# Kernel optimization log

Hardware: AMD Instinct MI355X
Metric: run time of the kernel (lower is better)

## Reference

```python
import jax, jax.numpy as jnp
import numpy as np
import math

B, S, D_IN, EMBED, H = 4, 1024, 1024, 1024, 16
HD = EMBED // H  # 64


def setup_inputs() -> dict:
    key = jax.random.key(0)
    ks = jax.random.split(key, 8)
    x = jax.random.normal(ks[0], (B, S, D_IN), dtype=jnp.float32)
    mask = jax.random.randint(ks[1], (B, S, S), 0, 2, dtype=jnp.int32)
    weights = jax.random.uniform(ks[2], (B, S, S), dtype=jnp.float32)
    # xavier-uniform-ish scale for projections
    lim_qkv = math.sqrt(6.0 / (D_IN + 3 * EMBED))
    lim_o = math.sqrt(6.0 / (EMBED + EMBED))
    W_qkv = jax.random.uniform(ks[3], (3 * EMBED, D_IN), minval=-lim_qkv, maxval=lim_qkv, dtype=jnp.float32)
    b_qkv = jnp.zeros((3 * EMBED,), dtype=jnp.float32)
    W_o = jax.random.uniform(ks[4], (EMBED, EMBED), minval=-lim_o, maxval=lim_o, dtype=jnp.float32)
    b_o = jnp.zeros((EMBED,), dtype=jnp.float32)
    return {"x": x, "mask": mask, "weights": weights, "W_qkv": W_qkv, "b_qkv": b_qkv, "W_o": W_o, "b_o": b_o}


def reference(x, mask, weights, W_qkv, b_qkv, W_o, b_o):
    b, s, _ = x.shape
    # QKV projection: [b, s, 3*EMBED] -> [b, H, s, 3*HD]
    qkv = (x @ W_qkv.T + b_qkv).reshape(b, s, H, 3 * HD).transpose(0, 2, 1, 3)
    q, k, v = jnp.split(qkv, 3, axis=-1)  # each [b, H, s, HD]
    logits = jnp.einsum('bhqd,bhkd->bhqk', q, k) / math.sqrt(HD)
    logits = jnp.where(mask[:, None, :, :] == 0, jnp.float32(-9e15), logits)
    # weights transposed on last two dims, broadcast over heads
    w = jnp.swapaxes(weights, -2, -1)[:, None, :, :]  # [b, 1, s, s]
    m = jnp.max(logits, axis=-1, keepdims=True)
    e = w * jnp.exp(logits - m)
    attn = e / jnp.sum(e, axis=-1, keepdims=True)
    vals = jnp.einsum('bhqk,bhkd->bhqd', attn, v)
    vals = vals.transpose(0, 2, 1, 3).reshape(b, s, EMBED)
    return vals @ W_o.T + b_o
```

## Files before the change

### kernel.cpp

```cpp
#include <hip/hip_runtime.h>
#include <hip/hip_bf16.h>
#include <stdint.h>

#define SDIM 1024
#define BATCH 4
#define NH 16
#define HDIM 64
#define KDIM 1024
#define N_QKV 3072
#define EMB 1024

typedef uint16_t u16;
typedef __attribute__((ext_vector_type(4))) float f32x4;
typedef __attribute__((ext_vector_type(8))) short bf16x8;
typedef __attribute__((ext_vector_type(8))) unsigned short u16x8;

__device__ __forceinline__ u16 f2bf(float f) {
  union { float f; uint32_t u; } x; x.f = f;
  uint32_t r = x.u + 0x7FFFu + ((x.u >> 16) & 1u);
  return (u16)(r >> 16);
}

__device__ __forceinline__ float bf2f(u16 b) {
  union { uint32_t u; float f; } x; x.u = ((uint32_t)b) << 16;
  return x.f;
}

__device__ __forceinline__ void gload_lds16(const u16* g, u16* l) {
  __builtin_amdgcn_global_load_lds(
      (const __attribute__((address_space(1))) unsigned int*)g,
      (__attribute__((address_space(3))) unsigned int*)l, 16, 0, 0);
}

#define N8_X  524288
#define N8_WQ 393216
#define N8_WO 131072
#define NCVT  1048576
#define NWM3  262144
__global__ void prep_kernel(const float* __restrict__ a, const float* __restrict__ bq,
                            const float* __restrict__ co,
                            u16* __restrict__ oa, u16* __restrict__ ob, u16* __restrict__ oc,
                            const int* __restrict__ mask, const float* __restrict__ wts,
                            u16* __restrict__ wm3) {
  const int total = NCVT + NWM3;
  const size_t SS = (size_t)SDIM * SDIM;
  int stride = gridDim.x * blockDim.x;
  for (int i = blockIdx.x * blockDim.x + threadIdx.x; i < total; i += stride) {
    if (i < NCVT) {
      const float* s; u16* d; int j;
      if (i < N8_X)             { s = a;  d = oa; j = i; }
      else if (i < N8_X + N8_WQ){ s = bq; d = ob; j = i - N8_X; }
      else                      { s = co; d = oc; j = i - N8_X - N8_WQ; }
      const float4* s4 = (const float4*)s + (size_t)j * 2;
      float4 u = s4[0], v = s4[1];
      u16x8 o;
      o[0] = f2bf(u.x); o[1] = f2bf(u.y); o[2] = f2bf(u.z); o[3] = f2bf(u.w);
      o[4] = f2bf(v.x); o[5] = f2bf(v.y); o[6] = f2bf(v.z); o[7] = f2bf(v.w);
      ((u16x8*)d)[j] = o;
    } else {
      int t = i - NCVT;
      int lane = t & 63, kt = (t >> 6) & 15, T = (t >> 10) & 63, b = t >> 16;
      int g2 = lane >> 4, c2 = lane & 15;
      int q = T * 16 + c2;
      const int* mrow = mask + (size_t)b * SS + (size_t)q * SDIM;
      const float* wcol = wts + (size_t)b * SS + q;
      u16* dst = wm3 + ((size_t)(b * 64 + T) * 16 + kt) * 1024 + lane * 16;
      #pragma unroll
      for (int hf = 0; hf < 2; ++hf) {
        int bk = kt * 64 + 8 * g2 + 32 * hf;
        int4 m0 = *(const int4*)(mrow + bk);
        int4 m1 = *(const int4*)(mrow + bk + 4);
        int mm[8] = {m0.x, m0.y, m0.z, m0.w, m1.x, m1.y, m1.z, m1.w};
        u16x8 o;
        #pragma unroll
        for (int e = 0; e < 8; ++e)
          o[e] = mm[e] ? f2bf(wcol[(size_t)(bk + e) * SDIM]) : (u16)0;
        *(u16x8*)(dst + hf * 8) = o;
      }
    }
  }
}

__global__ __launch_bounds__(512, 1) void gemm_qkv(
    const u16* __restrict__ A, const u16* __restrict__ Bm,
    const float* __restrict__ bias,
    u16* __restrict__ Qh, u16* __restrict__ Kh, u16* __restrict__ Vt)
{
  __shared__ char smem[114688];
  const int tid = threadIdx.x;
  const int gid = blockIdx.x;
  const int brow = (gid & 15) * 256, bcol = (gid >> 4) * 192;
  const int wid = tid >> 6, lane = tid & 63;
  const int g = lane >> 4, c = lane & 15, cx = c & 7;
  const int wr = wid & 3, wc = wid >> 2;

  const u16* asrc[4]; int adoff[4];
  #pragma unroll
  for (int j = 0; j < 4; ++j) {
    int i = j * 512 + tid;
    int row = i >> 3, sch = (i & 7) ^ (row & 7);
    asrc[j] = A + (size_t)(brow + row) * KDIM + sch * 8;
    adoff[j] = (j * 512 + wid * 64) * 16;
  }
  const u16* bsrc[3]; int bdoff[3];
  #pragma unroll
  for (int j = 0; j < 3; ++j) {
    int i = j * 512 + tid;
    int row = i >> 3, sch = (i & 7) ^ (row & 7);
    bsrc[j] = Bm + (size_t)(bcol + row) * KDIM + sch * 8;
    bdoff[j] = 32768 + (j * 512 + wid * 64) * 16;
  }

  auto stage = [&](int kt, int slot) {
    char* base = smem + slot * 57344;
    #pragma unroll
    for (int j = 0; j < 4; ++j)
      gload_lds16(asrc[j] + kt * 64, (u16*)(base + adoff[j]));
    #pragma unroll
    for (int j = 0; j < 3; ++j)
      gload_lds16(bsrc[j] + kt * 64, (u16*)(base + bdoff[j]));
  };

  f32x4 acc[4][6] = {};

  stage(0, 0);
  __syncthreads();

  for (int kt = 0; kt < 16; ++kt) {
    if (kt < 15) stage(kt + 1, (kt + 1) & 1);

    const char* As = smem + (kt & 1) * 57344;
    const char* Bs = As + 32768;

    #pragma unroll
    for (int kk = 0; kk < 2; ++kk) {
      bf16x8 af[4], bfr[6];
      #pragma unroll
      for (int m = 0; m < 4; ++m) {
        int row = wr * 64 + m * 16 + c;
        af[m] = *(const bf16x8*)(As + (row << 7) + ((((kk << 2) + g) ^ cx) << 4));
      }
      #pragma unroll
      for (int n = 0; n < 6; ++n) {
        int row = wc * 96 + n * 16 + c;
        bfr[n] = *(const bf16x8*)(Bs + (row << 7) + ((((kk << 2) + g) ^ cx) << 4));
      }
      __builtin_amdgcn_s_setprio(1);
      #pragma unroll
      for (int m = 0; m < 4; ++m)
        #pragma unroll
        for (int n = 0; n < 6; ++n)
          acc[m][n] = __builtin_amdgcn_mfma_f32_16x16x32_bf16(
              af[m], bfr[n], acc[m][n], 0, 0, 0);
      __builtin_amdgcn_s_setprio(0);
    }
    __syncthreads();
  }

  #pragma unroll
  for (int m = 0; m < 4; ++m) {
    #pragma unroll
    for (int n = 0; n < 6; ++n) {
      int col = bcol + wc * 96 + n * 16 + c;
      float bv = bias[col];
      int h = col / 192;
      int rem = col - h * 192;
      int sec = rem >> 6, d = rem & 63;
      #pragma unroll
      for (int r = 0; r < 4; ++r) {
        int row = brow + wr * 64 + m * 16 + g * 4 + r;
        int b = row >> 10, sl = row & 1023;
        float v = acc[m][n][r] + bv;
        if (sec == 0)
          Qh[((size_t)(b * NH + h) * SDIM + sl) * HDIM + d] = f2bf(v * 0.18033688f);
        else if (sec == 1)
          Kh[((size_t)(b * NH + h) * SDIM + sl) * HDIM + d] = f2bf(v);
        else
          Vt[((size_t)(b * NH + h) * HDIM + d) * SDIM + sl] = f2bf(v);
      }
    }
  }
}

__global__ __launch_bounds__(256) void gemm_bt(
    const u16* __restrict__ A, const u16* __restrict__ Bm,
    const float* __restrict__ bias, float* __restrict__ C,
    int M, int N, int K)
{
  __shared__ u16 As[128 * 64];
  __shared__ u16 Bs[128 * 64];
  const int tid = threadIdx.x;
  int bid = blockIdx.x;
  int swz = (bid & 7) * 32 + (bid >> 3);
  const int brow = (swz & 31) * 128, bcol = (swz >> 5) * 128;
  const int wid = tid >> 6, lane = tid & 63;
  const int g = lane >> 4, c = lane & 15, cx = c & 7;
  const int wrow = (wid >> 1) * 64, wcol = (wid & 1) * 64;

  const u16* asrc[4]; const u16* bsrc[4]; u16* adst[4]; u16* bdst[4];
  #pragma unroll
  for (int j = 0; j < 4; ++j) {
    int ci = j * 256 + tid;
    int row = ci >> 3, sch = (ci & 7) ^ (row & 7);
    asrc[j] = A  + (size_t)(brow + row) * K + sch * 8;
    bsrc[j] = Bm + (size_t)(bcol + row) * K + sch * 8;
    adst[j] = As + (j * 256 + wid * 64) * 8;
    bdst[j] = Bs + (j * 256 + wid * 64) * 8;
  }

  f32x4 acc[4][4] = {};
  const char* Asc = (const char*)As;
  const char* Bsc = (const char*)Bs;

  for (int kt = 0; kt < K / 64; ++kt) {
    #pragma unroll
    for (int j = 0; j < 4; ++j) {
      gload_lds16(asrc[j] + kt * 64, adst[j]);
      gload_lds16(bsrc[j] + kt * 64, bdst[j]);
    }
    __syncthreads();

    bf16x8 af[2][4], bfr[2][4];
    #pragma unroll
    for (int kk = 0; kk < 2; ++kk)
      #pragma unroll
      for (int i = 0; i < 4; ++i) {
        int cha = ((kk << 2) + g) ^ cx;
        af[kk][i]  = *(const bf16x8*)(Asc + ((wrow + i * 16 + c) << 7) + (cha << 4));
        bfr[kk][i] = *(const bf16x8*)(Bsc + ((wcol + i * 16 + c) << 7) + (cha << 4));
      }
    #pragma unroll
    for (int kk = 0; kk < 2; ++kk)
      #pragma unroll
      for (int mi = 0; mi < 4; ++mi)
        #pragma unroll
        for (int ni = 0; ni < 4; ++ni)
          acc[mi][ni] = __builtin_amdgcn_mfma_f32_16x16x32_bf16(
              af[kk][mi], bfr[kk][ni], acc[mi][ni], 0, 0, 0);
    __syncthreads();
  }

  #pragma unroll
  for (int mi = 0; mi < 4; ++mi)
    #pragma unroll
    for (int ni = 0; ni < 4; ++ni) {
      int col = bcol + wcol + ni * 16 + c;
      float bv = bias[col];
      #pragma unroll
      for (int r = 0; r < 4; ++r) {
        int row = brow + wrow + mi * 16 + g * 4 + r;
        C[(size_t)row * N + col] = acc[mi][ni][r] + bv;
      }
    }
}

__global__ __launch_bounds__(256, 4) void attn_kernel(
    const u16* __restrict__ Qh, const u16* __restrict__ Kh, const u16* __restrict__ Vt,
    const u16* __restrict__ wm3, u16* __restrict__ vals)
{
  int bid = blockIdx.x;
  int swz = (bid & 7) * 128 + (bid >> 3);
  const int qt = swz & 15, bh = swz >> 4;
  const int h = bh & 15, b = bh >> 4;

  const int tid = threadIdx.x;
  const int wid = tid >> 6, lane = tid & 63;
  const int g = lane >> 4, c = lane & 15;
  const int qloc = qt * 64 + wid * 16;

  __shared__ u16 Kb[2][4096];
  __shared__ u16 Vb[2][4096];

  const u16* qp = Qh + ((size_t)bh * SDIM + qloc + c) * HDIM;
  bf16x8 qa0 = *(const bf16x8*)(qp + g * 8);
  bf16x8 qa1 = *(const bf16x8*)(qp + 32 + g * 8);

  const u16* kbase = Kh + (size_t)bh * SDIM * HDIM;
  const u16* vbase = Vt + (size_t)bh * HDIM * SDIM;
  const u16* wbase = wm3 + (((size_t)(b * 16 + qt) * 4 + wid) * 16) * 1024 + lane * 16;

  float l_run = 0.f;
  f32x4 acc_o[4] = {};

  auto fsw = [](int row) { return ((row ^ (row >> 3)) & 7) ^ ((row & 1) << 2); };

  int kro[4], kxr[4], vro[4], vxr[4];
  #pragma unroll
  for (int st = 0; st < 4; ++st) {
    int kr = ((c >> 2) << 3) + ((st & 1) << 2) + (c & 3) + ((st >> 1) << 5);
    kro[st] = kr << 7;
    kxr[st] = fsw(kr);
  }
  #pragma unroll
  for (int dt = 0; dt < 4; ++dt) {
    int vr = dt * 16 + c;
    vro[dt] = vr << 7;
    vxr[dt] = fsw(vr);
  }

  auto stage = [&](int buf, int kt) {
    const int k0 = kt * 64;
    #pragma unroll
    for (int j = 0; j < 2; ++j) {
      int i = j * 256 + tid;
      int row = i >> 3;
      int sch = (i & 7) ^ (((row ^ (row >> 3)) & 7) ^ ((row & 1) << 2));
      gload_lds16(kbase + (size_t)(k0 + row) * HDIM + sch * 8,
                  &Kb[buf][(size_t)(j * 256 + wid * 64) * 8]);
      gload_lds16(vbase + (size_t)row * SDIM + k0 + sch * 8,
                  &Vb[buf][(size_t)(j * 256 + wid * 64) * 8]);
    }
  };

  stage(0, 0);
  __syncthreads();
  int cur = 0;

  for (int kt = 0; kt < 16; ++kt) {
    if (kt < 15) stage(cur ^ 1, kt + 1);

    u16x8 w0 = *(const u16x8*)(wbase + kt * 1024);
    u16x8 w1 = *(const u16x8*)(wbase + kt * 1024 + 8);

    const char* kb = (const char*)&Kb[cur][0];
    const char* vb = (const char*)&Vb[cur][0];

    f32x4 sc[4];
    #pragma unroll
    for (int st = 0; st < 4; ++st) {
      bf16x8 ka0 = *(const bf16x8*)(kb + kro[st] + ((g ^ kxr[st]) << 4));
      bf16x8 ka1 = *(const bf16x8*)(kb + kro[st] + (((4 + g) ^ kxr[st]) << 4));
      f32x4 z = {};
      z = __builtin_amdgcn_mfma_f32_16x16x32_bf16(ka0, qa0, z, 0, 0, 0);
      z = __builtin_amdgcn_mfma_f32_16x16x32_bf16(ka1, qa1, z, 0, 0, 0);
      sc[st] = z;
    }

    float p[4][4];
    #pragma unroll
    for (int st = 0; st < 4; ++st) {
      #pragma unroll
      for (int r = 0; r < 4; ++r) {
        u16 wv = (st < 2) ? ((const u16*)&w0)[st * 4 + r]
                          : ((const u16*)&w1)[(st - 2) * 4 + r];
        float pv = bf2f(wv) * __builtin_amdgcn_exp2f(sc[st][r]);
        p[st][r] = pv;
        l_run += pv;
      }
    }

    uint32_t pk[8];
    #pragma unroll
    for (int i = 0; i < 8; ++i) {
      float lo = p[i >> 1][(i & 1) * 2], hi = p[i >> 1][(i & 1) * 2 + 1];
      asm("v_cvt_pk_bf16_f32 %0, %1, %2" : "=v"(pk[i]) : "v"(lo), "v"(hi));
    }
    union PA { uint32_t u[4]; bf16x8 v; } a0, a1;
    #pragma unroll
    for (int i = 0; i < 4; ++i) { a0.u[i] = pk[i]; a1.u[i] = pk[4 + i]; }

    #pragma unroll
    for (int dt = 0; dt < 4; ++dt) {
      bf16x8 vb0 = *(const bf16x8*)(vb + vro[dt] + ((g ^ vxr[dt]) << 4));
      bf16x8 vb1 = *(const bf16x8*)(vb + vro[dt] + (((4 + g) ^ vxr[dt]) << 4));
      acc_o[dt] = __builtin_amdgcn_mfma_f32_16x16x32_bf16(a0.v, vb0, acc_o[dt], 0, 0, 0);
      acc_o[dt] = __builtin_amdgcn_mfma_f32_16x16x32_bf16(a1.v, vb1, acc_o[dt], 0, 0, 0);
    }

    __syncthreads();
    cur ^= 1;
  }

  l_run += __shfl_xor(l_run, 16);
  l_run += __shfl_xor(l_run, 32);

  float inv[4];
  #pragma unroll
  for (int r = 0; r < 4; ++r)
    inv[r] = 1.0f / __shfl(l_run, g * 4 + r);

  #pragma unroll
  for (int dt = 0; dt < 4; ++dt)
    #pragma unroll
    for (int r = 0; r < 4; ++r) {
      int row = b * SDIM + qloc + g * 4 + r;
      vals[(size_t)row * EMB + h * HDIM + dt * 16 + c] = f2bf(acc_o[dt][r] * inv[r]);
    }
}

extern "C" void kernel_launch(void* const* d_in, const int* in_sizes, int n_in,
                              void* d_out, int out_size, void* d_ws, size_t ws_size,
                              hipStream_t stream) {
  const float* x     = (const float*)d_in[0];
  const int*   mask  = (const int*)d_in[1];
  const float* wts   = (const float*)d_in[2];
  const float* W_qkv = (const float*)d_in[3];
  const float* b_qkv = (const float*)d_in[4];
  const float* W_o   = (const float*)d_in[5];
  const float* b_o   = (const float*)d_in[6];
  float* out = (float*)d_out;

  char* ws = (char*)d_ws;
  u16* xb   = (u16*)(ws);
  u16* wqb  = (u16*)(ws + (8ull  << 20));
  u16* wob  = (u16*)(ws + (14ull << 20));
  u16* Qh   = (u16*)(ws + (16ull << 20));
  u16* Kh   = (u16*)(ws + (24ull << 20));
  u16* Vt   = (u16*)(ws + (32ull << 20));
  u16* valb = (u16*)(ws + (40ull << 20));
  u16* wm3b = (u16*)d_out;

  prep_kernel<<<2048, 256, 0, stream>>>(x, W_qkv, W_o, xb, wqb, wob, mask, wts, wm3b);

  gemm_qkv<<<256, 512, 0, stream>>>(xb, wqb, b_qkv, Qh, Kh, Vt);

  attn_kernel<<<1024, 256, 0, stream>>>(Qh, Kh, Vt, wm3b, valb);

  gemm_bt<<<256, 256, 0, stream>>>(valb, wob, b_o, out, BATCH * SDIM, EMB, KDIM);
}
```

Measured before the change: 108.1 us.

## Overlap mask/weights prep and W_o conversion with QKV GEMM via extra warps

Moves the mask-times-weights packing and the W_o bf16 conversion out of the prep kernel into four extra wavefronts of the QKV GEMM block. Those wavefronts do the memory-bound prep work while the other eight run the MFMA GEMM, sharing its barriers so the two can overlap. The block grows to 768 threads, which adds register pressure, and the extra waves' memory traffic can contend with the GEMM's loads. The launch bound of 3 blocks per SM cannot be met given the 112 KB of shared memory per block.

```diff
diff --git a/kernel.cpp b/kernel.cpp
--- a/kernel.cpp
+++ b/kernel.cpp
@@ -34,150 +34,164 @@
 
 #define N8_X  524288
 #define N8_WQ 393216
-#define N8_WO 131072
-#define NCVT  1048576
-#define NWM3  262144
+#define NCVT2 917504
 __global__ void prep_kernel(const float* __restrict__ a, const float* __restrict__ bq,
-                            const float* __restrict__ co,
-                            u16* __restrict__ oa, u16* __restrict__ ob, u16* __restrict__ oc,
-                            const int* __restrict__ mask, const float* __restrict__ wts,
-                            u16* __restrict__ wm3) {
-  const int total = NCVT + NWM3;
-  const size_t SS = (size_t)SDIM * SDIM;
+                            u16* __restrict__ oa, u16* __restrict__ ob) {
   int stride = gridDim.x * blockDim.x;
-  for (int i = blockIdx.x * blockDim.x + threadIdx.x; i < total; i += stride) {
-    if (i < NCVT) {
-      const float* s; u16* d; int j;
-      if (i < N8_X)             { s = a;  d = oa; j = i; }
-      else if (i < N8_X + N8_WQ){ s = bq; d = ob; j = i - N8_X; }
-      else                      { s = co; d = oc; j = i - N8_X - N8_WQ; }
-      const float4* s4 = (const float4*)s + (size_t)j * 2;
-      float4 u = s4[0], v = s4[1];
-      u16x8 o;
-      o[0] = f2bf(u.x); o[1] = f2bf(u.y); o[2] = f2bf(u.z); o[3] = f2bf(u.w);
-      o[4] = f2bf(v.x); o[5] = f2bf(v.y); o[6] = f2bf(v.z); o[7] = f2bf(v.w);
-      ((u16x8*)d)[j] = o;
-    } else {
-      int t = i - NCVT;
-      int lane = t & 63, kt = (t >> 6) & 15, T = (t >> 10) & 63, b = t >> 16;
-      int g2 = lane >> 4, c2 = lane & 15;
-      int q = T * 16 + c2;
-      const int* mrow = mask + (size_t)b * SS + (size_t)q * SDIM;
-      const float* wcol = wts + (size_t)b * SS + q;
-      u16* dst = wm3 + ((size_t)(b * 64 + T) * 16 + kt) * 1024 + lane * 16;
-      #pragma unroll
-      for (int hf = 0; hf < 2; ++hf) {
-        int bk = kt * 64 + 8 * g2 + 32 * hf;
-        int4 m0 = *(const int4*)(mrow + bk);
-        int4 m1 = *(const int4*)(mrow + bk + 4);
-        int mm[8] = {m0.x, m0.y, m0.z, m0.w, m1.x, m1.y, m1.z, m1.w};
-        u16x8 o;
-        #pragma unroll
-        for (int e = 0; e < 8; ++e)
-          o[e] = mm[e] ? f2bf(wcol[(size_t)(bk + e) * SDIM]) : (u16)0;
-        *(u16x8*)(dst + hf * 8) = o;
-      }
-    }
-  }
-}
-
-__global__ __launch_bounds__(512, 1) void gemm_qkv(
+  for (int i = blockIdx.x * blockDim.x + threadIdx.x; i < NCVT2; i += stride) {
+    const float* s; u16* d; int j;
+    if (i < N8_X) { s = a;  d = oa; j = i; }
+    else          { s = bq; d = ob; j = i - N8_X; }
+    const float4* s4 = (const float4*)s + (size_t)j * 2;
+    float4 u = s4[0], v = s4[1];
+    u16x8 o;
+    o[0] = f2bf(u.x); o[1] = f2bf(u.y); o[2] = f2bf(u.z); o[3] = f2bf(u.w);
+    o[4] = f2bf(v.x); o[5] = f2bf(v.y); o[6] = f2bf(v.z); o[7] = f2bf(v.w);
+    ((u16x8*)d)[j] = o;
+  }
+}
+
+__global__ __launch_bounds__(768, 3) void gemm_qkv_fused(
     const u16* __restrict__ A, const u16* __restrict__ Bm,
     const float* __restrict__ bias,
-    u16* __restrict__ Qh, u16* __restrict__ Kh, u16* __restrict__ Vt)
+    u16* __restrict__ Qh, u16* __restrict__ Kh, u16* __restrict__ Vt,
+    const int* __restrict__ mask, const float* __restrict__ wts,
+    u16* __restrict__ wm3, const float* __restrict__ wo_f32, u16* __restrict__ wob)
 {
   __shared__ char smem[114688];
   const int tid = threadIdx.x;
   const int gid = blockIdx.x;
-  const int brow = (gid & 15) * 256, bcol = (gid >> 4) * 192;
-  const int wid = tid >> 6, lane = tid & 63;
-  const int g = lane >> 4, c = lane & 15, cx = c & 7;
-  const int wr = wid & 3, wc = wid >> 2;
-
-  const u16* asrc[4]; int adoff[4];
-  #pragma unroll
-  for (int j = 0; j < 4; ++j) {
-    int i = j * 512 + tid;
-    int row = i >> 3, sch = (i & 7) ^ (row & 7);
-    asrc[j] = A + (size_t)(brow + row) * KDIM + sch * 8;
-    adoff[j] = (j * 512 + wid * 64) * 16;
-  }
-  const u16* bsrc[3]; int bdoff[3];
-  #pragma unroll
-  for (int j = 0; j < 3; ++j) {
-    int i = j * 512 + tid;
-    int row = i >> 3, sch = (i & 7) ^ (row & 7);
-    bsrc[j] = Bm + (size_t)(bcol + row) * KDIM + sch * 8;
-    bdoff[j] = 32768 + (j * 512 + wid * 64) * 16;
-  }
-
-  auto stage = [&](int kt, int slot) {
-    char* base = smem + slot * 57344;
-    #pragma unroll
-    for (int j = 0; j < 4; ++j)
-      gload_lds16(asrc[j] + kt * 64, (u16*)(base + adoff[j]));
-    #pragma unroll
-    for (int j = 0; j < 3; ++j)
-      gload_lds16(bsrc[j] + kt * 64, (u16*)(base + bdoff[j]));
-  };
-
-  f32x4 acc[4][6] = {};
-
-  stage(0, 0);
-  __syncthreads();
-
-  for (int kt = 0; kt < 16; ++kt) {
-    if (kt < 15) stage(kt + 1, (kt + 1) & 1);
-
-    const char* As = smem + (kt & 1) * 57344;
-    const char* Bs = As + 32768;
-
-    #pragma unroll
-    for (int kk = 0; kk < 2; ++kk) {
-      bf16x8 af[4], bfr[6];
-      #pragma unroll
-      for (int m = 0; m < 4; ++m) {
-        int row = wr * 64 + m * 16 + c;
-        af[m] = *(const bf16x8*)(As + (row << 7) + ((((kk << 2) + g) ^ cx) << 4));
-      }
+
+  if (tid < 512) {
+    const int brow = (gid & 15) * 256, bcol = (gid >> 4) * 192;
+    const int wid = tid >> 6, lane = tid & 63;
+    const int g = lane >> 4, c = lane & 15, cx = c & 7;
+    const int wr = wid & 3, wc = wid >> 2;
+
+    const u16* asrc[4]; int adoff[4];
+    #pragma unroll
+    for (int j = 0; j < 4; ++j) {
+      int i = j * 512 + tid;
+      int row = i >> 3, sch = (i & 7) ^ (row & 7);
+      asrc[j] = A + (size_t)(brow + row) * KDIM + sch * 8;
+      adoff[j] = (j * 512 + wid * 64) * 16;
+    }
+    const u16* bsrc[3]; int bdoff[3];
+    #pragma unroll
+    for (int j = 0; j < 3; ++j) {
+      int i = j * 512 + tid;
+      int row = i >> 3, sch = (i & 7) ^ (row & 7);
+      bsrc[j] = Bm + (size_t)(bcol + row) * KDIM + sch * 8;
+      bdoff[j] = 32768 + (j * 512 + wid * 64) * 16;
+    }
+
+    auto stage = [&](int kt, int slot) {
+      char* base = smem + slot * 57344;
+      #pragma unroll
+      for (int j = 0; j < 4; ++j)
+        gload_lds16(asrc[j] + kt * 64, (u16*)(base + adoff[j]));
+      #pragma unroll
+      for (int j = 0; j < 3; ++j)
+        gload_lds16(bsrc[j] + kt * 64, (u16*)(base + bdoff[j]));
+    };
+
+    f32x4 acc[4][6] = {};
+
+    stage(0, 0);
+    __syncthreads();
+
+    for (int kt = 0; kt < 16; ++kt) {
+      if (kt < 15) stage(kt + 1, (kt + 1) & 1);
+
+      const char* As = smem + (kt & 1) * 57344;
+      const char* Bs = As + 32768;
+
+      #pragma unroll
+      for (int kk = 0; kk < 2; ++kk) {
+        bf16x8 af[4], bfr[6];
+        #pragma unroll
+        for (int m = 0; m < 4; ++m) {
+          int row = wr * 64 + m * 16 + c;
+          af[m] = *(const bf16x8*)(As + (row << 7) + ((((kk << 2) + g) ^ cx) << 4));
+        }
+        #pragma unroll
+        for (int n = 0; n < 6; ++n) {
+          int row = wc * 96 + n * 16 + c;
+          bfr[n] = *(const bf16x8*)(Bs + (row << 7) + ((((kk << 2) + g) ^ cx) << 4));
+        }
+        __builtin_amdgcn_s_setprio(1);
+        #pragma unroll
+        for (int m = 0; m < 4; ++m)
+          #pragma unroll
+          for (int n = 0; n < 6; ++n)
+            acc[m][n] = __builtin_amdgcn_mfma_f32_16x16x32_bf16(
+                af[m], bfr[n], acc[m][n], 0, 0, 0);
+        __builtin_amdgcn_s_setprio(0);
+      }
+      __syncthreads();
+    }
+
+    #pragma unroll
+    for (int m = 0; m < 4; ++m) {
       #pragma unroll
       for (int n = 0; n < 6; ++n) {
-        int row = wc * 96 + n * 16 + c;
-        bfr[n] = *(const bf16x8*)(Bs + (row << 7) + ((((kk << 2) + g) ^ cx) << 4));
-      }
-      __builtin_amdgcn_s_setprio(1);
-      #pragma unroll
-      for (int m = 0; m < 4; ++m)
-        #pragma unroll
-        for (int n = 0; n < 6; ++n)
-          acc[m][n] = __builtin_amdgcn_mfma_f32_16x16x32_bf16(
-              af[m], bfr[n], acc[m][n], 0, 0, 0);
-      __builtin_amdgcn_s_setprio(0);
-    }
+        int col = bcol + wc * 96 + n * 16 + c;
+        float bv = bias[col];
+        int h = col / 192;
+        int rem = col - h * 192;
+        int sec = rem >> 6, d = rem & 63;
+        #pragma unroll
+        for (int r = 0; r < 4; ++r) {
+          int row = brow + wr * 64 + m * 16 + g * 4 + r;
+          int b = row >> 10, sl = row & 1023;
+          float v = acc[m][n][r] + bv;
+          if (sec == 0)
+            Qh[((size_t)(b * NH + h) * SDIM + sl) * HDIM + d] = f2bf(v * 0.18033688f);
+          else if (sec == 1)
+            Kh[((size_t)(b * NH + h) * SDIM + sl) * HDIM + d] = f2bf(v);
+          else
+            Vt[((size_t)(b * NH + h) * HDIM + d) * SDIM + sl] = f2bf(v);
+        }
+      }
+    }
+  } else {
+    const int atid = tid - 512;
+    const int atg = gid * 256 + atid;
+    const size_t SS = (size_t)SDIM * SDIM;
+
     __syncthreads();
-  }
-
-  #pragma unroll
-  for (int m = 0; m < 4; ++m) {
-    #pragma unroll
-    for (int n = 0; n < 6; ++n) {
-      int col = bcol + wc * 96 + n * 16 + c;
-      float bv = bias[col];
-      int h = col / 192;
-      int rem = col - h * 192;
-      int sec = rem >> 6, d = rem & 63;
-      #pragma unroll
-      for (int r = 0; r < 4; ++r) {
-        int row = brow + wr * 64 + m * 16 + g * 4 + r;
-        int b = row >> 10, sl = row & 1023;
-        float v = acc[m][n][r] + bv;
-        if (sec == 0)
-          Qh[((size_t)(b * NH + h) * SDIM + sl) * HDIM + d] = f2bf(v * 0.18033688f);
-        else if (sec == 1)
-          Kh[((size_t)(b * NH + h) * SDIM + sl) * HDIM + d] = f2bf(v);
-        else
-          Vt[((size_t)(b * NH + h) * HDIM + d) * SDIM + sl] = f2bf(v);
-      }
+
+    for (int kt = 0; kt < 16; ++kt) {
+      if ((kt & 3) == 0) {
+        const int b = kt >> 2;
+        const int lane = atg & 63, ktw = (atg >> 6) & 15, T = (atg >> 10) & 63;
+        const int g2 = lane >> 4, c2 = lane & 15;
+        const int q = T * 16 + c2;
+        const int* mrow = mask + (size_t)b * SS + (size_t)q * SDIM;
+        const float* wcol = wts + (size_t)b * SS + q;
+        u16* dst = wm3 + ((size_t)(b * 64 + T) * 16 + ktw) * 1024 + lane * 16;
+        #pragma unroll
+        for (int hf = 0; hf < 2; ++hf) {
+          int bk = ktw * 64 + 8 * g2 + 32 * hf;
+          int4 m0 = *(const int4*)(mrow + bk);
+          int4 m1 = *(const int4*)(mrow + bk + 4);
+          int mm[8] = {m0.x, m0.y, m0.z, m0.w, m1.x, m1.y, m1.z, m1.w};
+          u16x8 o;
+          #pragma unroll
+          for (int e = 0; e < 8; ++e)
+            o[e] = mm[e] ? f2bf(wcol[(size_t)(bk + e) * SDIM]) : (u16)0;
+          *(u16x8*)(dst + hf * 8) = o;
+        }
+      } else if (kt == 2 || kt == 6) {
+        int u = ((kt == 6) ? 65536 : 0) + atg;
+        const float4* s4 = (const float4*)wo_f32 + (size_t)u * 2;
+        float4 uu = s4[0], v = s4[1];
+        u16x8 o;
+        o[0] = f2bf(uu.x); o[1] = f2bf(uu.y); o[2] = f2bf(uu.z); o[3] = f2bf(uu.w);
+        o[4] = f2bf(v.x);  o[5] = f2bf(v.y);  o[6] = f2bf(v.z);  o[7] = f2bf(v.w);
+        ((u16x8*)wob)[u] = o;
+      }
+      __syncthreads();
     }
   }
 }
@@ -410,9 +424,10 @@
   u16* valb = (u16*)(ws + (40ull << 20));
   u16* wm3b = (u16*)d_out;
 
-  prep_kernel<<<2048, 256, 0, stream>>>(x, W_qkv, W_o, xb, wqb, wob, mask, wts, wm3b);
-
-  gemm_qkv<<<256, 512, 0, stream>>>(xb, wqb, b_qkv, Qh, Kh, Vt);
+  prep_kernel<<<2048, 256, 0, stream>>>(x, W_qkv, xb, wqb);
+
+  gemm_qkv_fused<<<256, 768, 0, stream>>>(xb, wqb, b_qkv, Qh, Kh, Vt,
+                                          mask, wts, wm3b, W_o, wob);
 
   attn_kernel<<<1024, 256, 0, stream>>>(Qh, Kh, Vt, wm3b, valb);
 
```

Result: slower. 117.0 us (+8.2%).
